# Kernel optimization log

Hardware: AMD Instinct MI355X
Metric: run time of the kernel (lower is better)

Reference implementation:

```python
import jax, jax.numpy as jnp
import numpy as np

DIM = 512
NUM_HEADS = 16
HEAD_DIM = DIM // NUM_HEADS
HIDDEN = int(DIM * 4.0)
EPS = 1e-5


def layer_norm(x, gamma, beta):
    mu = jnp.mean(x, axis=-1, keepdims=True)
    var = jnp.mean(jnp.square(x - mu), axis=-1, keepdims=True)
    return (x - mu) * jax.lax.rsqrt(var + EPS) * gamma + beta


def setup_inputs() -> dict:
    key = jax.random.key(0)
    ks = jax.random.split(key, 8)
    B, L, C = 32, 3136, DIM
    x = jax.random.normal(ks[0], (B, L, C), dtype=jnp.float32)
    norm1_g = jnp.ones((C,), jnp.float32)
    norm1_b = jnp.zeros((C,), jnp.float32)
    # spatial (per-head) mixing weight: (num_heads, head_dim, head_dim)
    w_spatial = jax.random.normal(ks[1], (NUM_HEADS, HEAD_DIM, HEAD_DIM), jnp.float32) * (1.0 / np.sqrt(HEAD_DIM))
    norm2_g = jnp.ones((C,), jnp.float32)
    norm2_b = jnp.zeros((C,), jnp.float32)
    w1 = jax.random.normal(ks[2], (C, HIDDEN), jnp.float32) * (1.0 / np.sqrt(C))
    b1 = jnp.zeros((HIDDEN,), jnp.float32)
    w2 = jax.random.normal(ks[3], (HIDDEN, C), jnp.float32) * (1.0 / np.sqrt(HIDDEN))
    b2 = jnp.zeros((C,), jnp.float32)
    return {"x": x, "norm1_g": norm1_g, "norm1_b": norm1_b, "w_spatial": w_spatial,
            "norm2_g": norm2_g, "norm2_b": norm2_b, "w1": w1, "b1": b1, "w2": w2, "b2": b2}


def reference(x, norm1_g, norm1_b, w_spatial, norm2_g, norm2_b, w1, b1, w2, b2):
    B, L, C = x.shape
    shortcut = x
    h = layer_norm(x, norm1_g, norm1_b)
    # window partition -> per-head channel-sub-dim linear (shared across windows/positions)
    # mathematically equivalent to applying the per-head matmul at every token
    h = h.reshape(B, L, NUM_HEADS, HEAD_DIM)
    h = jnp.einsum('blhd,hde->blhe', h, w_spatial)
    h = h.reshape(B, L, C)
    x = shortcut + h
    # channel MLP: Linear -> GELU(tanh) -> Linear
    y = layer_norm(x, norm2_g, norm2_b)
    y = jax.nn.gelu(y @ w1 + b1, approximate=True)
    y = y @ w2 + b2
    return x + y
```

## Files before the change

### kernel.cpp

```cpp
#include <hip/hip_runtime.h>
#include <hip/hip_bf16.h>


typedef __bf16 bf16x8 __attribute__((ext_vector_type(8)));
typedef float f32x16 __attribute__((ext_vector_type(16)));

constexpr int CDIM = 512;
constexpr int HID = 2048;
constexpr int MROWS = 32 * 3136;
constexpr float LN_EPS = 1e-5f;

static __device__ __forceinline__ float gelu_tanh(float x) {
  const float u = 0.7978845608028654f * fmaf(0.044715f * x * x, x, x);
  const float e = __expf(2.0f * u);
  return 0.5f * x * (2.0f - 2.0f / (e + 1.0f));
}

static __device__ __forceinline__ void load_lds16(const void* g, void* l) {
  __builtin_amdgcn_global_load_lds((__attribute__((address_space(1))) void*)g,
                                   (__attribute__((address_space(3))) void*)l,
                                   16, 0, 0);
}

template <int KD, int ND>
__global__ __launch_bounds__(256) void cvt_pack32(
    const float* __restrict__ src, __hip_bfloat16* __restrict__ dst) {
  constexpr int NKT2 = KD / 16;
  const int o = blockIdx.x * 256 + threadIdx.x;
  const int l = o & 63;
  const int gt = o >> 6;
  const int t = gt & (NKT2 - 1), g = gt / NKT2;
  const int n = g * 32 + (l & 31);
  const int k0 = t * 16 + (l >> 5) * 8;
  __hip_bfloat16 v[8];
#pragma unroll
  for (int j = 0; j < 8; ++j)
    v[j] = __float2bfloat16(src[(size_t)(k0 + j) * ND + n]);
  *(uint4*)(dst + (size_t)o * 8) = *(const uint4*)v;
}

__global__ __launch_bounds__(256) void fused_pre(
    const float* __restrict__ x, const float* __restrict__ g1,
    const float* __restrict__ b1, const float* __restrict__ wsp,
    const float* __restrict__ g2, const float* __restrict__ b2,
    float* __restrict__ x2out, __hip_bfloat16* __restrict__ yout) {
  __shared__ float lnbuf[4][CDIM];
  __shared__ float red[4][4][2];

  const int t = threadIdx.x;
  const int lane = t & 63;
  const int w = t >> 6;
  const int c0 = 2 * t;
  const int hd = c0 >> 5, e0 = c0 & 31;
  const int ypc32 = (c0 >> 4) * 512 + ((c0 >> 3) & 1) * 256 + (c0 & 7);

  float wc0[32], wc1[32];
#pragma unroll
  for (int d = 0; d < 32; ++d) {
    const float2 wv = *(const float2*)&wsp[(hd * 32 + d) * 32 + e0];
    wc0[d] = wv.x;
    wc1[d] = wv.y;
  }
  const float2 g1v = *(const float2*)&g1[c0];
  const float2 b1v = *(const float2*)&b1[c0];
  const float2 g2v = *(const float2*)&g2[c0];
  const float2 b2v = *(const float2*)&b2[c0];

  for (int rq = blockIdx.x; rq < MROWS / 4; rq += gridDim.x) {
    const size_t r0 = (size_t)rq * 4;
    float2 xv[4];
#pragma unroll
    for (int r = 0; r < 4; ++r)
      xv[r] = *(const float2*)&x[(r0 + r) * CDIM + c0];

    float s[4], q[4];
#pragma unroll
    for (int r = 0; r < 4; ++r) {
      s[r] = xv[r].x + xv[r].y;
      q[r] = xv[r].x * xv[r].x + xv[r].y * xv[r].y;
    }
#pragma unroll
    for (int off = 32; off; off >>= 1)
#pragma unroll
      for (int r = 0; r < 4; ++r) {
        s[r] += __shfl_down(s[r], off);
        q[r] += __shfl_down(q[r], off);
      }
    if (lane == 0)
#pragma unroll
      for (int r = 0; r < 4; ++r) {
        red[w][r][0] = s[r];
        red[w][r][1] = q[r];
      }
    __syncthreads();
    float mu[4], rs[4];
#pragma unroll
    for (int r = 0; r < 4; ++r) {
      s[r] = red[0][r][0] + red[1][r][0] + red[2][r][0] + red[3][r][0];
      q[r] = red[0][r][1] + red[1][r][1] + red[2][r][1] + red[3][r][1];
      mu[r] = s[r] * (1.0f / CDIM);
      rs[r] = rsqrtf(q[r] * (1.0f / CDIM) - mu[r] * mu[r] + LN_EPS);
      lnbuf[r][c0] = (xv[r].x - mu[r]) * rs[r] * g1v.x + b1v.x;
      lnbuf[r][c0 + 1] = (xv[r].y - mu[r]) * rs[r] * g1v.y + b1v.y;
    }
    __syncthreads();

    float h[4][2] = {};
#pragma unroll
    for (int d = 0; d < 32; ++d) {
#pragma unroll
      for (int r = 0; r < 4; ++r) {
        const float lv = lnbuf[r][hd * 32 + d];
        h[r][0] = fmaf(lv, wc0[d], h[r][0]);
        h[r][1] = fmaf(lv, wc1[d], h[r][1]);
      }
    }
    float a[4][2];
#pragma unroll
    for (int r = 0; r < 4; ++r) {
      a[r][0] = xv[r].x + h[r][0];
      a[r][1] = xv[r].y + h[r][1];
      float2 av;
      av.x = a[r][0];
      av.y = a[r][1];
      *(float2*)&x2out[(r0 + r) * CDIM + c0] = av;
      s[r] = a[r][0] + a[r][1];
      q[r] = a[r][0] * a[r][0] + a[r][1] * a[r][1];
    }
#pragma unroll
    for (int off = 32; off; off >>= 1)
#pragma unroll
      for (int r = 0; r < 4; ++r) {
        s[r] += __shfl_down(s[r], off);
        q[r] += __shfl_down(q[r], off);
      }
    if (lane == 0)
#pragma unroll
      for (int r = 0; r < 4; ++r) {
        red[w][r][0] = s[r];
        red[w][r][1] = q[r];
      }
    __syncthreads();
#pragma unroll
    for (int r = 0; r < 4; ++r) {
      s[r] = red[0][r][0] + red[1][r][0] + red[2][r][0] + red[3][r][0];
      q[r] = red[0][r][1] + red[1][r][1] + red[2][r][1] + red[3][r][1];
      mu[r] = s[r] * (1.0f / CDIM);
      rs[r] = rsqrtf(q[r] * (1.0f / CDIM) - mu[r] * mu[r] + LN_EPS);
      __hip_bfloat162 yv;
      yv.x = __float2bfloat16((a[r][0] - mu[r]) * rs[r] * g2v.x + b2v.x);
      yv.y = __float2bfloat16((a[r][1] - mu[r]) * rs[r] * g2v.y + b2v.y);
      const size_t rr = r0 + r;
      *(__hip_bfloat162*)&yout[(rr >> 5) * 16384 + (rr & 31) * 8 + ypc32] = yv;
    }
    __syncthreads();
  }
}

template <int K, int N, bool GELU, int GM>
__global__ __launch_bounds__(256, 4) void gemm32p(
    const char* __restrict__ Ap, const char* __restrict__ Bp,
    const float* __restrict__ bias, char* __restrict__ zp,
    float* __restrict__ fout) {
  constexpr int NT = N / 128;
  constexpr int NKT2A = K / 16;
  constexpr int NKT2 = K / 16;
  constexpr int NST = K / 32;
  __shared__ __attribute__((aligned(16))) char smem[32768];

  const int tid = threadIdx.x;
  const int lane = tid & 63;
  const int w = tid >> 6;
  const int wr = w >> 1, wc = w & 1;

  const int cpx = gridDim.x >> 3;
  const int lid = (blockIdx.x & 7) * cpx + (blockIdx.x >> 3);
  constexpr int CHUNK = GM * NT;
  const int ch = lid / CHUNK, idx = lid - ch * CHUNK;
  const int tn = idx / GM;
  const int tm = ch * GM + (idx - tn * GM);
  const size_t am0 = (size_t)tm * 128;
  const int bn0 = tn * 128;

  const size_t aBlk0 =
      ((size_t)(tm * 4 + (tid >> 7)) * NKT2A + ((tid >> 6) & 1));
  const size_t aBlk1 = aBlk0 + (size_t)2 * NKT2A;
  const char* aP0 = Ap + aBlk0 * 1024 + lane * 16;
  const char* aP1 = Ap + aBlk1 * 1024 + lane * 16;
  const int ldsA0 = (tid >> 6) * 1024;
  const int ldsA1 = 4096 + (tid >> 6) * 1024;

  const char* bBase =
      Bp + ((size_t)(tn * 4 + wc * 2) * NKT2) * 1024 + lane * 16;

#define STAGE_A(so, kt)                                         \
  do {                                                          \
    load_lds16(aP0 + (size_t)(kt) * 2048, smem + (so) + ldsA0); \
    load_lds16(aP1 + (size_t)(kt) * 2048, smem + (so) + ldsA1); \
  } while (0)

  f32x16 acc[2][2] = {};
  bf16x8 bf[2][2], bfn[2][2], af[2][2];

  STAGE_A(0, 0);
#pragma unroll
  for (int ni = 0; ni < 2; ++ni)
#pragma unroll
    for (int kh = 0; kh < 2; ++kh)
      bf[ni][kh] = *(const bf16x8*)(bBase + ((size_t)ni * NKT2 + kh) * 1024);
  __syncthreads();

  for (int t = 0; t < NST; ++t) {
    const int d = (t & 1) * 8192, dn = 8192 - d;
    if (t + 1 < NST) {
      STAGE_A(dn, t + 1);
#pragma unroll
      for (int ni = 0; ni < 2; ++ni)
#pragma unroll
        for (int kh = 0; kh < 2; ++kh)
          bfn[ni][kh] =
              *(const bf16x8*)(bBase +
                               ((size_t)ni * NKT2 + 2 * (t + 1) + kh) * 1024);
    }

#pragma unroll
    for (int mi = 0; mi < 2; ++mi)
#pragma unroll
      for (int kh = 0; kh < 2; ++kh)
        af[mi][kh] = *(const bf16x8*)(smem + d +
                                      ((wr * 2 + mi) * 2 + kh) * 1024 +
                                      lane * 16);
#pragma unroll
    for (int kh = 0; kh < 2; ++kh)
#pragma unroll
      for (int mi = 0; mi < 2; ++mi)
#pragma unroll
        for (int ni = 0; ni < 2; ++ni)
          acc[mi][ni] = __builtin_amdgcn_mfma_f32_32x32x16_bf16(
              af[mi][kh], bf[ni][kh], acc[mi][ni], 0, 0, 0);
    if (t + 1 < NST) {
#pragma unroll
      for (int ni = 0; ni < 2; ++ni)
#pragma unroll
        for (int kh = 0; kh < 2; ++kh) bf[ni][kh] = bfn[ni][kh];
    }
    __syncthreads();
  }
#undef STAGE_A

  const int ccol = lane & 31;
  const int rbase = 4 * (lane >> 5);
  char* smb = smem;

  if constexpr (GELU) {
#pragma unroll
    for (int ni = 0; ni < 2; ++ni) {
      const int col = wc * 64 + ni * 32 + ccol;
      const float bv = bias[bn0 + col];
      const int cpart =
          (col >> 4) * 1024 + ((col >> 3) & 1) * 512 + (col & 7) * 2;
#pragma unroll
      for (int mi = 0; mi < 2; ++mi)
#pragma unroll
        for (int r = 0; r < 16; ++r) {
          const int row = wr * 64 + mi * 32 + (r & 3) + 8 * (r >> 2) + rbase;
          *(__hip_bfloat16*)(smb + (row >> 5) * 8192 + (row & 31) * 16 +
                             cpart) =
              __float2bfloat16(gelu_tanh(acc[mi][ni][r] + bv));
        }
    }
    __syncthreads();
#pragma unroll
    for (int it = 0; it < 8; ++it) {
      const int seg = it * 256 + tid;
      const int blk = seg >> 6, l = seg & 63;
      const size_t gb =
          ((size_t)(am0 >> 5) + (blk >> 3)) * (N / 16) + (bn0 >> 4) + (blk & 7);
      *(uint4*)(zp + gb * 1024 + l * 16) = *(const uint4*)(smb + seg * 16);
    }
  } else {
    float* ot = (float*)smb;
#pragma unroll
    for (int p = 0; p < 2; ++p) {
      if (p) __syncthreads();
      if (wr == p) {
#pragma unroll
        for (int ni = 0; ni < 2; ++ni) {
          const int col = wc * 64 + ni * 32 + ccol;
          const float bv = bias[bn0 + col];
#pragma unroll
          for (int mi = 0; mi < 2; ++mi)
#pragma unroll
            for (int r = 0; r < 16; ++r) {
              const int rl = mi * 32 + (r & 3) + 8 * (r >> 2) + rbase;
              ot[rl * 128 + col] = acc[mi][ni][r] + bv;
            }
        }
      }
      __syncthreads();
#pragma unroll
      for (int it = 0; it < 8; ++it) {
        const int seg = it * 256 + tid;
        const int row = seg >> 5, cs = seg & 31;
        const float4 lv = *(const float4*)(smb + seg * 16);
        float* gp = &fout[(am0 + p * 64 + row) * N + bn0 + cs * 4];
        float4 o = *(const float4*)gp;
        o.x += lv.x;
        o.y += lv.y;
        o.z += lv.z;
        o.w += lv.w;
        *(float4*)gp = o;
      }
    }
  }
}

extern "C" void kernel_launch(void* const* d_in, const int* in_sizes, int n_in,
                              void* d_out, int out_size, void* d_ws,
                              size_t ws_size, hipStream_t stream) {
  const float* x = (const float*)d_in[0];
  const float* n1g = (const float*)d_in[1];
  const float* n1b = (const float*)d_in[2];
  const float* wsp = (const float*)d_in[3];
  const float* n2g = (const float*)d_in[4];
  const float* n2b = (const float*)d_in[5];
  const float* w1 = (const float*)d_in[6];
  const float* b1 = (const float*)d_in[7];
  const float* w2 = (const float*)d_in[8];
  const float* b2 = (const float*)d_in[9];
  float* out = (float*)d_out;

  __hip_bfloat16* ybuf = (__hip_bfloat16*)d_ws;
  __hip_bfloat16* zbuf = ybuf + (size_t)MROWS * CDIM;
  __hip_bfloat16* w1p = zbuf + (size_t)MROWS * HID;
  __hip_bfloat16* w2p = w1p + (size_t)CDIM * HID;

  cvt_pack32<CDIM, HID><<<512, 256, 0, stream>>>(w1, w1p);
  cvt_pack32<HID, CDIM><<<512, 256, 0, stream>>>(w2, w2p);
  fused_pre<<<2048, 256, 0, stream>>>(x, n1g, n1b, wsp, n2g, n2b, out, ybuf);
  gemm32p<CDIM, HID, true, 8><<<(MROWS / 128) * (HID / 128), 256, 0, stream>>>(
      (const char*)ybuf, (const char*)w1p, b1, (char*)zbuf, nullptr);
  gemm32p<HID, CDIM, false, 1>
      <<<(MROWS / 128) * (CDIM / 128), 256, 0, stream>>>(
          (const char*)zbuf, (const char*)w2p, b2, nullptr, out);
}
```

Measured before the change: 835.4 us.

## Stage A tiles per wave privately in LDS to drop block barriers

In both MLP GEMMs, each wave now copies its own A sub-tile into a private LDS region, so wave pairs sharing rows each load the same data. This removes the per-iteration __syncthreads; explicit s_waitcnt vmcnt counts plus a sched_barrier now guarantee that the async global-to-LDS copies have landed before they are read. The LDS double buffer grows to fill the 32 KB allocation, and the launch-bounds occupancy hint drops from 4 to 3 blocks. The cost is doubled A traffic from L2 into LDS and tighter register and LDS pressure, traded for less barrier stalling.

```diff
diff --git a/kernel.cpp b/kernel.cpp
--- a/kernel.cpp
+++ b/kernel.cpp
@@ -158,7 +158,7 @@
 }
 
 template <int K, int N, bool GELU, int GM>
-__global__ __launch_bounds__(256, 4) void gemm32p(
+__global__ __launch_bounds__(256, 3) void gemmwp(
     const char* __restrict__ Ap, const char* __restrict__ Bp,
     const float* __restrict__ bias, char* __restrict__ zp,
     float* __restrict__ fout) {
@@ -182,21 +182,20 @@
   const size_t am0 = (size_t)tm * 128;
   const int bn0 = tn * 128;
 
-  const size_t aBlk0 =
-      ((size_t)(tm * 4 + (tid >> 7)) * NKT2A + ((tid >> 6) & 1));
-  const size_t aBlk1 = aBlk0 + (size_t)2 * NKT2A;
-  const char* aP0 = Ap + aBlk0 * 1024 + lane * 16;
-  const char* aP1 = Ap + aBlk1 * 1024 + lane * 16;
-  const int ldsA0 = (tid >> 6) * 1024;
-  const int ldsA1 = 4096 + (tid >> 6) * 1024;
+  const char* aG[2];
+  aG[0] = Ap + ((size_t)(tm * 4 + wr * 2) * NKT2A) * 1024 + lane * 16;
+  aG[1] = Ap + ((size_t)(tm * 4 + wr * 2 + 1) * NKT2A) * 1024 + lane * 16;
+  const int myBase = w * 4096;
 
   const char* bBase =
       Bp + ((size_t)(tn * 4 + wc * 2) * NKT2) * 1024 + lane * 16;
 
-#define STAGE_A(so, kt)                                         \
-  do {                                                          \
-    load_lds16(aP0 + (size_t)(kt) * 2048, smem + (so) + ldsA0); \
-    load_lds16(aP1 + (size_t)(kt) * 2048, smem + (so) + ldsA1); \
+#define STAGE_A(so, t1)                                                       \
+  do {                                                                        \
+    _Pragma("unroll") for (int mi = 0; mi < 2; ++mi)                          \
+        _Pragma("unroll") for (int kh = 0; kh < 2; ++kh)                      \
+            load_lds16(aG[mi] + (size_t)(2 * (t1) + kh) * 1024,               \
+                       smem + (so) + myBase + (mi * 2 + kh) * 1024);          \
   } while (0)
 
   f32x16 acc[2][2] = {};
@@ -208,12 +207,10 @@
 #pragma unroll
     for (int kh = 0; kh < 2; ++kh)
       bf[ni][kh] = *(const bf16x8*)(bBase + ((size_t)ni * NKT2 + kh) * 1024);
-  __syncthreads();
 
   for (int t = 0; t < NST; ++t) {
-    const int d = (t & 1) * 8192, dn = 8192 - d;
+    const int d = (t & 1) * 16384, dn = 16384 - d;
     if (t + 1 < NST) {
-      STAGE_A(dn, t + 1);
 #pragma unroll
       for (int ni = 0; ni < 2; ++ni)
 #pragma unroll
@@ -221,15 +218,22 @@
           bfn[ni][kh] =
               *(const bf16x8*)(bBase +
                                ((size_t)ni * NKT2 + 2 * (t + 1) + kh) * 1024);
-    }
+      STAGE_A(dn, t + 1);
+    }
+    if (t == 0)
+      asm volatile("s_waitcnt vmcnt(12)" ::: "memory");
+    else if (t == NST - 1)
+      asm volatile("s_waitcnt vmcnt(0)" ::: "memory");
+    else
+      asm volatile("s_waitcnt vmcnt(8)" ::: "memory");
+    __builtin_amdgcn_sched_barrier(0);
 
 #pragma unroll
     for (int mi = 0; mi < 2; ++mi)
 #pragma unroll
       for (int kh = 0; kh < 2; ++kh)
-        af[mi][kh] = *(const bf16x8*)(smem + d +
-                                      ((wr * 2 + mi) * 2 + kh) * 1024 +
-                                      lane * 16);
+        af[mi][kh] = *(const bf16x8*)(smem + d + myBase +
+                                      (mi * 2 + kh) * 1024 + lane * 16);
 #pragma unroll
     for (int kh = 0; kh < 2; ++kh)
 #pragma unroll
@@ -244,9 +248,10 @@
 #pragma unroll
         for (int kh = 0; kh < 2; ++kh) bf[ni][kh] = bfn[ni][kh];
     }
-    __syncthreads();
   }
 #undef STAGE_A
+
+  __syncthreads();
 
   const int ccol = lane & 31;
   const int rbase = 4 * (lane >> 5);
@@ -338,9 +343,9 @@
   cvt_pack32<CDIM, HID><<<512, 256, 0, stream>>>(w1, w1p);
   cvt_pack32<HID, CDIM><<<512, 256, 0, stream>>>(w2, w2p);
   fused_pre<<<2048, 256, 0, stream>>>(x, n1g, n1b, wsp, n2g, n2b, out, ybuf);
-  gemm32p<CDIM, HID, true, 8><<<(MROWS / 128) * (HID / 128), 256, 0, stream>>>(
+  gemmwp<CDIM, HID, true, 8><<<(MROWS / 128) * (HID / 128), 256, 0, stream>>>(
       (const char*)ybuf, (const char*)w1p, b1, (char*)zbuf, nullptr);
-  gemm32p<HID, CDIM, false, 1>
+  gemmwp<HID, CDIM, false, 1>
       <<<(MROWS / 128) * (CDIM / 128), 256, 0, stream>>>(
           (const char*)zbuf, (const char*)w2p, b2, nullptr, out);
 }
```

After: 933.1 us. +11.7%, slower.
